# Performance work log

Measured on AMD Instinct MI355X. Metric: run time of the kernel, lower is better.

## Reference

```python
import jax, jax.numpy as jnp
import numpy as np

B, ST, SK, D, H, HD, MLP, BLK, NRAND = 2, 2048, 2048, 512, 8, 64, 2048, 64, 3


def _bigbird_block_mask(nq, nk, r, rng):
    """Block-level BigBird mask: 3-block window + global first/last blocks + r random blocks/row."""
    bm = np.zeros((nq, nk), dtype=bool)
    for i in range(nq):
        bm[i, max(i - 1, 0):min(i + 2, nk)] = True  # sliding window of 3 blocks
    bm[0, :] = True; bm[-1, :] = True              # global query blocks
    bm[:, 0] = True; bm[:, -1] = True              # global key blocks
    for i in range(nq):
        avail = np.where(~bm[i])[0]
        if avail.size:
            bm[i, rng.choice(avail, size=min(r, avail.size), replace=False)] = True
    return bm


def _masks():
    rng = np.random.RandomState(0)  # connectivity_seed = 0
    nb_q, nb_k = ST // BLK, SK // BLK
    self_bm = _bigbird_block_mask(nb_q, nb_q, NRAND, rng)
    cross_bm = _bigbird_block_mask(nb_q, nb_k, NRAND, rng)
    ones_blk = np.ones((BLK, BLK), dtype=bool)
    self_mask = np.kron(self_bm, ones_blk) & np.tril(np.ones((ST, ST), dtype=bool))  # causal self-attn
    cross_mask = np.kron(cross_bm, ones_blk)
    return jnp.asarray(self_mask), jnp.asarray(cross_mask)


def setup_inputs() -> dict:
    key = jax.random.key(0)
    ks = jax.random.split(key, 12)
    sd = np.float32(1.0 / np.sqrt(D))
    sh = np.float32(1.0 / np.sqrt(H * HD))
    sm = np.float32(1.0 / np.sqrt(MLP))
    self_mask, cross_mask = _masks()
    return dict(
        targets=jax.random.normal(ks[0], (B, ST, D), jnp.float32),
        encoded=jax.random.normal(ks[1], (B, SK, D), jnp.float32),
        ln1_scale=jnp.ones((D,), jnp.float32), ln1_bias=jnp.zeros((D,), jnp.float32),
        ln2_scale=jnp.ones((D,), jnp.float32), ln2_bias=jnp.zeros((D,), jnp.float32),
        ln3_scale=jnp.ones((D,), jnp.float32), ln3_bias=jnp.zeros((D,), jnp.float32),
        wq1=jax.random.normal(ks[2], (D, H, HD), jnp.float32) * sd,
        wk1=jax.random.normal(ks[3], (D, H, HD), jnp.float32) * sd,
        wv1=jax.random.normal(ks[4], (D, H, HD), jnp.float32) * sd,
        wo1=jax.random.normal(ks[5], (H, HD, D), jnp.float32) * sh,
        wq2=jax.random.normal(ks[6], (D, H, HD), jnp.float32) * sd,
        wk2=jax.random.normal(ks[7], (D, H, HD), jnp.float32) * sd,
        wv2=jax.random.normal(ks[8], (D, H, HD), jnp.float32) * sd,
        wo2=jax.random.normal(ks[9], (H, HD, D), jnp.float32) * sh,
        mlp_w1=jax.random.normal(ks[10], (D, MLP), jnp.float32) * sd,
        mlp_b1=jnp.zeros((MLP,), jnp.float32),
        mlp_w2=jax.random.normal(ks[11], (MLP, D), jnp.float32) * sm,
        mlp_b2=jnp.zeros((D,), jnp.float32),
        self_mask=self_mask, cross_mask=cross_mask,
    )


def _ln(x, s, b, eps=1e-6):
    mu = jnp.mean(x, axis=-1, keepdims=True)
    var = jnp.mean(jnp.square(x - mu), axis=-1, keepdims=True)
    return (x - mu) * jax.lax.rsqrt(var + eps) * s + b


def _attn(xq, xkv, wq, wk, wv, wo, mask):
    q = jnp.einsum('bsd,dhk->bshk', xq, wq) * np.float32(1.0 / np.sqrt(HD))
    k = jnp.einsum('bsd,dhk->bshk', xkv, wk)
    v = jnp.einsum('bsd,dhk->bshk', xkv, wv)
    scores = jnp.einsum('bqhd,bkhd->bhqk', q, k)
    scores = jnp.where(mask[None, None], scores, jnp.float32(-1e9))
    w = jax.nn.softmax(scores, axis=-1)
    o = jnp.einsum('bhqk,bkhd->bqhd', w, v)
    return jnp.einsum('bqhd,hdo->bqo', o, wo)


def reference(targets, encoded, ln1_scale, ln1_bias, ln2_scale, ln2_bias, ln3_scale, ln3_bias,
              wq1, wk1, wv1, wo1, wq2, wk2, wv2, wo2,
              mlp_w1, mlp_b1, mlp_w2, mlp_b2, self_mask, cross_mask):
    # causal BigBird self-attention + residual
    x = _ln(targets, ln1_scale, ln1_bias)
    x = _attn(x, x, wq1, wk1, wv1, wo1, self_mask) + targets
    # BigBird cross-attention over encoder output + residual
    y = _ln(x, ln2_scale, ln2_bias)
    y = _attn(y, encoded, wq2, wk2, wv2, wo2, cross_mask) + x
    # MLP block + residual
    z = _ln(y, ln3_scale, ln3_bias)
    z = jax.nn.gelu(z @ mlp_w1 + mlp_b1) @ mlp_w2 + mlp_b2
    return y + z
```

## Files before the change

### kernel.cpp

```cpp
#include <hip/hip_runtime.h>
#include <hip/hip_bf16.h>

#define DEVINL __device__ __forceinline__

namespace {

constexpr int kB = 2, kST = 2048, kSK = 2048, kD = 512, kH = 8, kHD = 64, kMLP = 2048, kBLK = 64;
constexpr int kNBQ = kST / kBLK;
constexpr int kNBK = kSK / kBLK;
constexpr int kROWS = kB * kST;
constexpr int kSPL = 8;

typedef float f32x4 __attribute__((ext_vector_type(4)));
typedef int i32x4 __attribute__((ext_vector_type(4)));
typedef short bf16x8 __attribute__((ext_vector_type(8)));

DEVINL float bf2f(unsigned short u) { return __uint_as_float(((unsigned)u) << 16); }

DEVINL unsigned short f2bf(float f) {
  __hip_bfloat16 h = __float2bfloat16(f);
  return *reinterpret_cast<unsigned short*>(&h);
}

DEVINL f32x4 mfma16(bf16x8 a, bf16x8 b, f32x4 c) {
  return __builtin_amdgcn_mfma_f32_16x16x32_bf16(a, b, c, 0, 0, 0);
}

DEVINL int swzb(int r) { return (((r & 7) ^ ((r >> 3) & 7)) << 4); }

__global__ __launch_bounds__(256) void tobf_kernel(const void* __restrict__ src, unsigned short* __restrict__ dst,
                                                   int n8, const unsigned* __restrict__ probe) {
  const bool bf = (probe[0] == 0x3F803F80u);
  const int stride = gridDim.x * blockDim.x;
  if (bf) {
    const i32x4* s = (const i32x4*)src;
    i32x4* d = (i32x4*)dst;
    for (int i = blockIdx.x * blockDim.x + threadIdx.x; i < n8; i += stride) d[i] = s[i];
  } else {
    const f32x4* s = (const f32x4*)src;
    i32x4* d = (i32x4*)dst;
    for (int i = blockIdx.x * blockDim.x + threadIdx.x; i < n8; i += stride) {
      const f32x4 a = s[2 * i], c = s[2 * i + 1];
      union { i32x4 v; unsigned short u[8]; } pk;
#pragma unroll
      for (int j = 0; j < 4; j++) { pk.u[j] = f2bf(a[j]); pk.u[4 + j] = f2bf(c[j]); }
      d[i] = pk.v;
    }
  }
}

struct PSrc { const void* s[8]; };
__global__ __launch_bounds__(256) void param_cvt_kernel(PSrc ps, float* __restrict__ dst,
                                                        const unsigned* __restrict__ probe) {
  const bool bf = (probe[0] == 0x3F803F80u);
  const int i = blockIdx.x * blockDim.x + threadIdx.x;
  if (i >= 5632) return;
  int seg, off;
  if (i < 3072) { seg = i >> 9; off = i & 511; }
  else if (i < 5120) { seg = 6; off = i - 3072; }
  else { seg = 7; off = i - 5120; }
  dst[i] = bf ? bf2f(((const unsigned short*)ps.s[seg])[off]) : ((const float*)ps.s[seg])[off];
}

struct TDesc { const void* src; unsigned short* dst; int K, N, start; float alpha; };
struct TPack { TDesc d[10]; };

__global__ __launch_bounds__(256) void transpose_batch_kernel(TPack p, const unsigned* __restrict__ probe) {
  __shared__ float tile[32][33];
  const bool bf = (probe[0] == 0x3F803F80u);
  const int bid = blockIdx.x;
  int di = 0;
#pragma unroll
  for (int i = 1; i < 10; i++)
    if (bid >= p.d[i].start) di = i;
  const TDesc dd = p.d[di];
  const int local = bid - dd.start;
  const int gx = dd.N / 32;
  const int bx = (local % gx) * 32;
  const int by = (local / gx) * 32;
  const int tx = threadIdx.x & 31, ty = threadIdx.x >> 5;
#pragma unroll
  for (int j = 0; j < 4; j++) {
    const int kr = by + ty + j * 8;
    float v;
    if (bf) v = bf2f(((const unsigned short*)dd.src)[(size_t)kr * dd.N + bx + tx]);
    else v = ((const float*)dd.src)[(size_t)kr * dd.N + bx + tx];
    tile[ty + j * 8][tx] = v;
  }
  __syncthreads();
#pragma unroll
  for (int j = 0; j < 4; j++) {
    const int nr = bx + ty + j * 8;
    dd.dst[(size_t)nr * dd.K + by + tx] = f2bf(dd.alpha * tile[tx][ty + j * 8]);
  }
}

DEVINL int mask_fmt(const void* self_mask) {
  const unsigned* sw = (const unsigned*)self_mask;
  unsigned w = sw[32256];
  unsigned w0 = sw[0];
  if (w == 0x01010101u) return 0;
  if (w0 == 0x3F800000u) return 2;
  if (w0 == 0x00003F80u) return 3;
  return 1;
}

DEVINL bool mask_at(const void* m, int r, int c, int fmt) {
  size_t idx = (size_t)r * kSK + c;
  switch (fmt) {
    case 0: return ((const unsigned char*)m)[idx] != 0;
    case 2: return ((const float*)m)[idx] != 0.f;
    case 3: return ((const unsigned short*)m)[idx] != 0;
    default: return ((const int*)m)[idx] != 0;
  }
}

__global__ void mask_kernel(const void* __restrict__ smask, const void* __restrict__ cmask,
                            unsigned char* __restrict__ sbm, unsigned char* __restrict__ cbm) {
  int fmt = mask_fmt(smask);
  int t = blockIdx.x * blockDim.x + threadIdx.x;
  if (t < kNBQ * kNBK) {
    int i = t / kNBK, j = t % kNBK;
    sbm[t] = mask_at(smask, i * kBLK + kBLK - 1, j * kBLK, fmt) ? 1 : 0;
    cbm[t] = mask_at(cmask, i * kBLK, j * kBLK, fmt) ? 1 : 0;
  }
}

__global__ __launch_bounds__(256) void ln_kernel(const void* __restrict__ x, const float* __restrict__ s,
                                                 const float* __restrict__ b, unsigned short* __restrict__ out,
                                                 int raw, const unsigned* __restrict__ probe) {
  const int row = blockIdx.x, t = threadIdx.x;
  float v0, v1;
  if (raw && probe[0] == 0x3F803F80u) {
    const unsigned u = ((const unsigned*)x)[(size_t)row * 256 + t];
    v0 = bf2f((unsigned short)u);
    v1 = bf2f((unsigned short)(u >> 16));
  } else {
    const float2 f = ((const float2*)x)[(size_t)row * 256 + t];
    v0 = f.x; v1 = f.y;
  }
  float sum = v0 + v1;
#pragma unroll
  for (int o = 32; o; o >>= 1) sum += __shfl_xor(sum, o);
  __shared__ float red[4], red2[4];
  const int wid = t >> 6, lane = t & 63;
  if (lane == 0) red[wid] = sum;
  __syncthreads();
  const float mu = (red[0] + red[1] + red[2] + red[3]) * (1.f / 512.f);
  float d0 = v0 - mu, d1 = v1 - mu;
  float vs = d0 * d0 + d1 * d1;
#pragma unroll
  for (int o = 32; o; o >>= 1) vs += __shfl_xor(vs, o);
  if (lane == 0) red2[wid] = vs;
  __syncthreads();
  const float rstd = rsqrtf((red2[0] + red2[1] + red2[2] + red2[3]) * (1.f / 512.f) + 1e-6f);
  const float o0 = d0 * rstd * s[2 * t] + b[2 * t];
  const float o1 = d1 * rstd * s[2 * t + 1] + b[2 * t + 1];
  ((unsigned*)out)[(size_t)row * 256 + t] = (unsigned)f2bf(o0) | ((unsigned)f2bf(o1) << 16);
}

DEVINL float gelu_f(float x) {
  float u = 0.7978845608028654f * (x + 0.044715f * x * x * x);
  return 0.5f * x * (1.f + tanhf(u));
}

enum { GEPI_QKV = 0, GEPI_QKV2 = 1, GEPI_RESID_RAW = 2, GEPI_RESID = 3, GEPI_GELU = 4, GEPI_FINAL = 5 };

template <int BM, int WM, int WN, int MT, int NT, int EPI>
__global__ __launch_bounds__(256) void mfma_gemm_kernel(
    const unsigned short* __restrict__ A, const unsigned short* __restrict__ A2,
    const unsigned short* __restrict__ Bt,
    void* __restrict__ Cout, int M, int N, int K,
    const float* __restrict__ bias, const void* __restrict__ resid,
    const unsigned* __restrict__ probe) {
  __shared__ __align__(16) unsigned short As[2][BM * 64];
  __shared__ __align__(16) unsigned short Bs[2][128 * 64];
  const int t = threadIdx.x, w = t >> 6, lane = t & 63;
  const int lg = lane >> 4, lc = lane & 15;
  const int wm = w / WN, wn = w % WN;
  const int bm = blockIdx.y * BM, bn = blockIdx.x * 128;

  const unsigned short* Aop = A;
  if constexpr (EPI == GEPI_QKV2) {
    if (bn >= 512) Aop = A2;
  }

  f32x4 acc[MT][NT];
#pragma unroll
  for (int mt = 0; mt < MT; mt++)
#pragma unroll
    for (int nt = 0; nt < NT; nt++) acc[mt][nt] = f32x4{0.f, 0.f, 0.f, 0.f};

  constexpr int AU = BM / 32;
  const int row0 = t >> 3, part16 = (t & 7) * 16;

  i32x4 ar[AU], br[4];
  auto LOADR = [&](int k0) {
#pragma unroll
    for (int i = 0; i < AU; i++) ar[i] = *(const i32x4*)(Aop + (size_t)(bm + row0 + i * 32) * K + k0 + (part16 >> 1));
#pragma unroll
    for (int i = 0; i < 4; i++) br[i] = *(const i32x4*)(Bt + (size_t)(bn + row0 + i * 32) * K + k0 + (part16 >> 1));
  };
  auto WRITES = [&](int buf) {
#pragma unroll
    for (int i = 0; i < AU; i++) {
      const int r = row0 + i * 32;
      *(i32x4*)((char*)&As[buf][0] + r * 128 + (part16 ^ swzb(r))) = ar[i];
    }
#pragma unroll
    for (int i = 0; i < 4; i++) {
      const int r = row0 + i * 32;
      *(i32x4*)((char*)&Bs[buf][0] + r * 128 + (part16 ^ swzb(r))) = br[i];
    }
  };
  auto COMPUTE = [&](int buf) {
#pragma unroll
    for (int c = 0; c < 2; c++) {
      bf16x8 af[MT], bfv[NT];
#pragma unroll
      for (int mt = 0; mt < MT; mt++) {
        const int r = wm * (MT * 16) + mt * 16 + lc;
        af[mt] = *(const bf16x8*)((const char*)&As[buf][0] + r * 128 + ((c * 64 + lg * 16) ^ swzb(r)));
      }
#pragma unroll
      for (int nt = 0; nt < NT; nt++) {
        const int r = wn * (NT * 16) + nt * 16 + lc;
        bfv[nt] = *(const bf16x8*)((const char*)&Bs[buf][0] + r * 128 + ((c * 64 + lg * 16) ^ swzb(r)));
      }
#pragma unroll
      for (int mt = 0; mt < MT; mt++)
#pragma unroll
        for (int nt = 0; nt < NT; nt++) acc[mt][nt] = mfma16(af[mt], bfv[nt], acc[mt][nt]);
    }
  };

  LOADR(0);
  WRITES(0);
  for (int k0 = 0; k0 < K; k0 += 128) {
    __syncthreads();
    LOADR(k0 + 64);
    COMPUTE(0);
    WRITES(1);
    __syncthreads();
    if (k0 + 128 < K) LOADR(k0 + 128);
    COMPUTE(1);
    if (k0 + 128 < K) WRITES(0);
  }

  bool prb = false;
  if constexpr (EPI == GEPI_FINAL || EPI == GEPI_RESID_RAW) prb = (probe[0] == 0x3F803F80u);
#pragma unroll
  for (int mt = 0; mt < MT; mt++) {
#pragma unroll
    for (int i = 0; i < 4; i++) {
      const int row = bm + wm * (MT * 16) + mt * 16 + lg * 4 + i;
#pragma unroll
      for (int nt = 0; nt < NT; nt++) {
        const int col = bn + wn * (NT * 16) + nt * 16 + lc;
        const float vv = acc[mt][nt][i];
        const size_t idx = (size_t)row * N + col;
        if constexpr (EPI == GEPI_QKV || EPI == GEPI_QKV2) {
          const int bb = row >> 11, ss = row & 2047;
          const int hh = (col >> 6) & 7, hd = col & 63;
          ((unsigned short*)Cout)[(size_t)(col >> 9) * kROWS * 512 +
                                  (((size_t)bb * kH + hh) * kST + ss) * 64 + hd] = f2bf(vv);
        } else if constexpr (EPI == GEPI_RESID_RAW) {
          const float rv = prb ? bf2f(((const unsigned short*)resid)[idx]) : ((const float*)resid)[idx];
          ((float*)Cout)[idx] = vv + rv;
        } else if constexpr (EPI == GEPI_RESID) {
          ((float*)Cout)[idx] = vv + ((const float*)resid)[idx];
        } else if constexpr (EPI == GEPI_GELU) {
          ((unsigned short*)Cout)[idx] = f2bf(gelu_f(vv + bias[col]));
        } else {
          const float r = vv + bias[col] + ((const float*)resid)[idx];
          if (prb) ((unsigned short*)Cout)[idx] = f2bf(r);
          else ((float*)Cout)[idx] = r;
        }
      }
    }
  }
}

template <bool CAUSAL>
__global__ __launch_bounds__(256) void attn_part_kernel(
    const unsigned short* __restrict__ q, const unsigned short* __restrict__ k,
    const unsigned short* __restrict__ v, const unsigned char* __restrict__ bm,
    unsigned short* __restrict__ opart, float* __restrict__ mpart, float* __restrict__ lpart) {
  __shared__ __align__(16) char smem[16384];
  const int x = blockIdx.x;
  const int s = x & 7, b = (x >> 3) & 1, qb = x >> 4;
  const int h = blockIdx.y;
  const int t = threadIdx.x, w = t >> 6, lane = t & 63;
  const int lg = lane >> 4, lc = lane & 15;

  const unsigned char* bmrow = bm + qb * kNBK;
  const unsigned mask = (unsigned)__ballot(lane < kNBK ? (bmrow[lane] != 0) : false);
  const int cnt = __popc(mask);
  const int lo = (s * cnt) >> 3, hi = ((s + 1) * cnt) >> 3;
  unsigned mrem = mask;
  for (int i = 0; i < lo; i++) mrem &= mrem - 1;
  const int left = hi - lo;

  const size_t hbase = ((size_t)b * kH + h) * kST;
  const size_t qbase = (hbase + qb * 64 + w * 16 + lc) * 64;
  const bf16x8 aq0 = *(const bf16x8*)(q + qbase + 8 * lg);
  const bf16x8 aq1 = *(const bf16x8*)(q + qbase + 32 + 8 * lg);

  f32x4 ob[4];
#pragma unroll
  for (int dt = 0; dt < 4; dt++) ob[dt] = f32x4{0.f, 0.f, 0.f, 0.f};
  float mi = -1e30f, li = 0.f;

  char* ksb = smem;
  char* vtb = smem + 8192;

  const int krr = t >> 3, kc16 = (t & 7) * 16;
  const int vkvp = t >> 3, vdc = (t & 7) * 8;
  const int vposb = ((vkvp >> 4) << 6) + (((vkvp >> 1) & 3) << 4) + (((vkvp >> 3) & 1) << 3) + ((vkvp & 1) << 2);

  i32x4 kr0, kr1, vr0, vr1;
  auto LOADT = [&](int j) {
    const unsigned short* kb = k + (hbase + j * 64) * 64;
    kr0 = *(const i32x4*)(kb + t * 8);
    kr1 = *(const i32x4*)(kb + 2048 + t * 8);
    const unsigned short* vb = v + (hbase + j * 64) * 64;
    vr0 = *(const i32x4*)(vb + (2 * vkvp) * 64 + vdc);
    vr1 = *(const i32x4*)(vb + (2 * vkvp + 1) * 64 + vdc);
  };
  auto WRITET = [&]() {
    *(i32x4*)(ksb + krr * 128 + (kc16 ^ swzb(krr))) = kr0;
    *(i32x4*)(ksb + (krr + 32) * 128 + (kc16 ^ swzb(krr + 32))) = kr1;
    union { i32x4 v4; unsigned short u[8]; } a0, a1;
    a0.v4 = vr0; a1.v4 = vr1;
#pragma unroll
    for (int jj = 0; jj < 8; jj++) {
      const int d = vdc + jj;
      const unsigned val = (unsigned)a0.u[jj] | ((unsigned)a1.u[jj] << 16);
      *(unsigned*)(vtb + d * 128 + (vposb ^ swzb(d))) = val;
    }
  };

  if (left > 0) {
    int jcur = (int)__builtin_ctz(mrem);
    mrem &= mrem - 1;
    LOADT(jcur);
    WRITET();
    for (int r = 0; r < left; r++) {
      int jnext = -1;
      if (r + 1 < left) { jnext = (int)__builtin_ctz(mrem); mrem &= mrem - 1; }
      __syncthreads();
      if (jnext >= 0) LOADT(jnext);

      f32x4 sv[4];
#pragma unroll
      for (int t4 = 0; t4 < 4; t4++) sv[t4] = f32x4{0.f, 0.f, 0.f, 0.f};
#pragma unroll
      for (int c = 0; c < 2; c++) {
        const bf16x8 aqc = c ? aq1 : aq0;
#pragma unroll
        for (int t4 = 0; t4 < 4; t4++) {
          const int row = t4 * 16 + lc;
          bf16x8 bk = *(const bf16x8*)(ksb + row * 128 + ((c * 64 + lg * 16) ^ swzb(row)));
          sv[t4] = mfma16(bk, aqc, sv[t4]);
        }
      }

      if (CAUSAL && jcur == qb) {
#pragma unroll
        for (int t4 = 0; t4 < 4; t4++)
#pragma unroll
          for (int i = 0; i < 4; i++)
            if (t4 * 16 + lg * 4 + i > w * 16 + lc) sv[t4][i] = -1e30f;
      }

      float pm = sv[0][0];
#pragma unroll
      for (int t4 = 0; t4 < 4; t4++)
#pragma unroll
        for (int i = 0; i < 4; i++) pm = fmaxf(pm, sv[t4][i]);
      pm = fmaxf(pm, __shfl_xor(pm, 16));
      pm = fmaxf(pm, __shfl_xor(pm, 32));
      const float mn = fmaxf(mi, pm);
      const float corr = __expf(mi - mn);
      mi = mn;
      float rs = 0.f;
#pragma unroll
      for (int t4 = 0; t4 < 4; t4++)
#pragma unroll
        for (int i = 0; i < 4; i++) {
          sv[t4][i] = __expf(sv[t4][i] - mn);
          rs += sv[t4][i];
        }
      rs += __shfl_xor(rs, 16);
      rs += __shfl_xor(rs, 32);
      li = li * corr + rs;

      float cb[4];
#pragma unroll
      for (int i = 0; i < 4; i++) cb[i] = __shfl(corr, lg * 4 + i);
#pragma unroll
      for (int dt = 0; dt < 4; dt++)
#pragma unroll
        for (int i = 0; i < 4; i++) ob[dt][i] *= cb[i];

      bf16x8 pa[2];
#pragma unroll
      for (int c = 0; c < 2; c++) {
        union { bf16x8 v8; unsigned short u[8]; } pk;
#pragma unroll
        for (int jj = 0; jj < 8; jj++) pk.u[jj] = f2bf(sv[2 * c + (jj >> 2)][jj & 3]);
        pa[c] = pk.v8;
      }
#pragma unroll
      for (int c = 0; c < 2; c++)
#pragma unroll
        for (int dt = 0; dt < 4; dt++) {
          const int row = dt * 16 + lc;
          bf16x8 bv = *(const bf16x8*)(vtb + row * 128 + ((c * 64 + lg * 16) ^ swzb(row)));
          ob[dt] = mfma16(pa[c], bv, ob[dt]);
        }

      __syncthreads();
      if (jnext >= 0) WRITET();
      jcur = jnext;
    }
  }

  const int pidx = ((((b * kNBQ + qb) * kH) + h)) * kSPL + s;
  unsigned short* op = opart + (size_t)pidx * 4096;
#pragma unroll
  for (int dt = 0; dt < 4; dt++)
#pragma unroll
    for (int i = 0; i < 4; i++)
      op[(w * 16 + lg * 4 + i) * 64 + dt * 16 + lc] = f2bf(ob[dt][i]);
  if (lg == 0) {
    mpart[pidx * 64 + w * 16 + lc] = mi;
    lpart[pidx * 64 + w * 16 + lc] = li;
  }
}

__global__ __launch_bounds__(256) void attn_comb_kernel(
    const unsigned short* __restrict__ opart, const float* __restrict__ mpart,
    const float* __restrict__ lpart, unsigned short* __restrict__ o) {
  const int x = blockIdx.x;
  const int qb = x >> 1, b = x & 1, h = blockIdx.y;
  const int t = threadIdx.x;
  const int base = ((((b * kNBQ + qb) * kH) + h)) * kSPL;
  const int r = t >> 2, cg = (t & 3) * 16;
  float m[kSPL], l[kSPL];
#pragma unroll
  for (int s = 0; s < kSPL; s++) {
    m[s] = mpart[(base + s) * 64 + r];
    l[s] = lpart[(base + s) * 64 + r];
  }
  float M = m[0];
#pragma unroll
  for (int s = 1; s < kSPL; s++) M = fmaxf(M, m[s]);
  float wgt[kSPL], L = 0.f;
#pragma unroll
  for (int s = 0; s < kSPL; s++) {
    wgt[s] = __expf(m[s] - M);
    L += l[s] * wgt[s];
  }
  const float inv = 1.f / L;
  float val[16];
#pragma unroll
  for (int c = 0; c < 16; c++) val[c] = 0.f;
#pragma unroll
  for (int s = 0; s < kSPL; s++) {
    const unsigned short* op = opart + (size_t)(base + s) * 4096 + r * 64 + cg;
    union { i32x4 v; unsigned short u[8]; } lo_, hi_;
    lo_.v = *(const i32x4*)op;
    hi_.v = *(const i32x4*)(op + 8);
#pragma unroll
    for (int c = 0; c < 8; c++) {
      val[c] += bf2f(lo_.u[c]) * wgt[s];
      val[8 + c] += bf2f(hi_.u[c]) * wgt[s];
    }
  }
  const size_t ob_ = (((size_t)b * kST + qb * 64 + r) * kH + h) * kHD + cg;
#pragma unroll
  for (int c = 0; c < 16; c++) o[ob_ + c] = f2bf(val[c] * inv);
}

}

extern "C" void kernel_launch(void* const* d_in, const int* in_sizes, int n_in,
                              void* d_out, int out_size, void* d_ws, size_t ws_size,
                              hipStream_t stream) {
  (void)in_sizes; (void)n_in; (void)out_size; (void)ws_size;
  const unsigned* probe = (const unsigned*)d_in[2];

  char* W = (char*)d_ws;
  size_t off = 0;
  auto allocb = [&](size_t bytes) { char* p = W + off; off += (bytes + 255) & ~size_t(255); return p; };

  float* xbuf = (float*)allocb((size_t)kROWS * kD * 4);
  float* ybuf = (float*)allocb((size_t)kROWS * kD * 4);
  float* f_par = (float*)allocb(5632 * 4);
  float* f_ln[6];
  for (int i = 0; i < 6; i++) f_ln[i] = f_par + i * 512;
  float* f_b1 = f_par + 3072;
  float* f_b2 = f_par + 5120;
  unsigned short* encb = (unsigned short*)allocb((size_t)kROWS * kD * 2);
  unsigned short* lnb  = (unsigned short*)allocb((size_t)kROWS * kD * 2);
  unsigned short* qkvb = (unsigned short*)allocb((size_t)3 * kROWS * kD * 2);
  unsigned short* qkv2 = (unsigned short*)allocb((size_t)3 * kROWS * kD * 2);
  unsigned short* aob  = (unsigned short*)allocb((size_t)kROWS * kD * 2);
  unsigned short* hb16 = (unsigned short*)allocb((size_t)kROWS * kMLP * 2);
  unsigned short* wqkv1 = (unsigned short*)allocb((size_t)3 * 512 * 512 * 2);
  unsigned short* wqkv2 = (unsigned short*)allocb((size_t)3 * 512 * 512 * 2);
  unsigned short* wo1t  = (unsigned short*)allocb((size_t)512 * 512 * 2);
  unsigned short* wo2t  = (unsigned short*)allocb((size_t)512 * 512 * 2);
  unsigned short* w1t   = (unsigned short*)allocb((size_t)2048 * 512 * 2);
  unsigned short* w2t   = (unsigned short*)allocb((size_t)512 * 2048 * 2);
  unsigned char* sbm = (unsigned char*)allocb(kNBQ * kNBK);
  unsigned char* cbm = (unsigned char*)allocb(kNBQ * kNBK);
  unsigned short* opart = (unsigned short*)allocb((size_t)512 * kSPL * 4096 * 2);
  float* mpart = (float*)allocb((size_t)512 * kSPL * 64 * 4);
  float* lpart = (float*)allocb((size_t)512 * kSPL * 64 * 4);

  tobf_kernel<<<1024, 256, 0, stream>>>(d_in[1], encb, kROWS * kD / 8, probe);
  {
    PSrc ps;
    for (int i = 0; i < 6; i++) ps.s[i] = d_in[2 + i];
    ps.s[6] = d_in[17];
    ps.s[7] = d_in[19];
    param_cvt_kernel<<<22, 256, 0, stream>>>(ps, f_par, probe);
  }
  {
    TPack p;
    const void* srcs[10] = {d_in[8], d_in[9], d_in[10],
                            d_in[12], d_in[13], d_in[14],
                            d_in[11], d_in[15], d_in[16], d_in[18]};
    unsigned short* dsts[10] = {wqkv1, wqkv1 + 512 * 512, wqkv1 + 2 * 512 * 512,
                                wqkv2, wqkv2 + 512 * 512, wqkv2 + 2 * 512 * 512,
                                wo1t, wo2t, w1t, w2t};
    const int Ksz[10] = {512, 512, 512, 512, 512, 512, 512, 512, 512, 2048};
    const int Nsz[10] = {512, 512, 512, 512, 512, 512, 512, 512, 2048, 512};
    int start = 0;
    for (int i = 0; i < 10; i++) {
      p.d[i].src = srcs[i]; p.d[i].dst = dsts[i]; p.d[i].K = Ksz[i]; p.d[i].N = Nsz[i];
      p.d[i].start = start;
      p.d[i].alpha = (i == 0 || i == 3) ? 0.125f : 1.0f;
      start += (Nsz[i] / 32) * (Ksz[i] / 32);
    }
    transpose_batch_kernel<<<start, 256, 0, stream>>>(p, probe);
  }
  mask_kernel<<<1, 1024, 0, stream>>>(d_in[20], d_in[21], sbm, cbm);

  const dim3 blk(256);
  const dim3 g_qkv(12, 32);
  const dim3 g_mlp1(16, 32);
  const dim3 g_n512(4, 64);
  const dim3 g_attnp(kNBQ * kB * kSPL, kH);
  const dim3 g_attnc(kNBQ * kB, kH);

  unsigned short* qb16 = qkvb;
  unsigned short* kb16 = qkvb + (size_t)kROWS * 512;
  unsigned short* vb16 = qkvb + (size_t)2 * kROWS * 512;
  unsigned short* q2b = qkv2;
  unsigned short* k2b = qkv2 + (size_t)kROWS * 512;
  unsigned short* v2b = qkv2 + (size_t)2 * kROWS * 512;

  ln_kernel<<<kROWS, blk, 0, stream>>>(d_in[0], f_ln[0], f_ln[1], lnb, 1, probe);
  mfma_gemm_kernel<128, 2, 2, 4, 4, GEPI_QKV><<<g_qkv, blk, 0, stream>>>(lnb, nullptr, wqkv1, qkvb, kROWS, 1536, 512, nullptr, nullptr, probe);
  attn_part_kernel<true><<<g_attnp, blk, 0, stream>>>(qb16, kb16, vb16, sbm, opart, mpart, lpart);
  attn_comb_kernel<<<g_attnc, blk, 0, stream>>>(opart, mpart, lpart, aob);
  mfma_gemm_kernel<64, 1, 4, 4, 2, GEPI_RESID_RAW><<<g_n512, blk, 0, stream>>>(aob, nullptr, wo1t, xbuf, kROWS, 512, 512, nullptr, d_in[0], probe);

  ln_kernel<<<kROWS, blk, 0, stream>>>(xbuf, f_ln[2], f_ln[3], lnb, 0, probe);
  mfma_gemm_kernel<128, 2, 2, 4, 4, GEPI_QKV2><<<g_qkv, blk, 0, stream>>>(lnb, encb, wqkv2, qkv2, kROWS, 1536, 512, nullptr, nullptr, probe);
  attn_part_kernel<false><<<g_attnp, blk, 0, stream>>>(q2b, k2b, v2b, cbm, opart, mpart, lpart);
  attn_comb_kernel<<<g_attnc, blk, 0, stream>>>(opart, mpart, lpart, aob);
  mfma_gemm_kernel<64, 1, 4, 4, 2, GEPI_RESID><<<g_n512, blk, 0, stream>>>(aob, nullptr, wo2t, ybuf, kROWS, 512, 512, nullptr, xbuf, probe);

  ln_kernel<<<kROWS, blk, 0, stream>>>(ybuf, f_ln[4], f_ln[5], lnb, 0, probe);
  mfma_gemm_kernel<128, 2, 2, 4, 4, GEPI_GELU><<<g_mlp1, blk, 0, stream>>>(lnb, nullptr, w1t, hb16, kROWS, kMLP, 512, f_b1, nullptr, probe);
  mfma_gemm_kernel<64, 1, 4, 4, 2, GEPI_FINAL><<<g_n512, blk, 0, stream>>>(hb16, nullptr, w2t, d_out, kROWS, 512, 2048, f_b2, ybuf, probe);
}
```

Measured before the change: 209.4 us.

## Merge prologue conversion kernels into one launch and swizzle GEMM workgroup order

Four setup kernels (encoder bf16 conversion, parameter conversion, weight transposes, block-mask extraction) are folded into a single prologue kernel that dispatches on block index. This removes three kernel launches and their serialization gaps. The GEMM kernel also remaps its flat workgroup index with a stride-8 permutation, so that consecutively dispatched workgroups spread across XCDs/tiles and get better L2 locality. The remap assumes the workgroup count divides by 8, which holds for the grids used.

Result: faster. 200.1 us (-4.4%).

```diff
diff --git a/kernel.cpp b/kernel.cpp
--- a/kernel.cpp
+++ b/kernel.cpp
@@ -28,72 +28,19 @@
 
 DEVINL int swzb(int r) { return (((r & 7) ^ ((r >> 3) & 7)) << 4); }
 
-__global__ __launch_bounds__(256) void tobf_kernel(const void* __restrict__ src, unsigned short* __restrict__ dst,
-                                                   int n8, const unsigned* __restrict__ probe) {
-  const bool bf = (probe[0] == 0x3F803F80u);
-  const int stride = gridDim.x * blockDim.x;
-  if (bf) {
-    const i32x4* s = (const i32x4*)src;
-    i32x4* d = (i32x4*)dst;
-    for (int i = blockIdx.x * blockDim.x + threadIdx.x; i < n8; i += stride) d[i] = s[i];
-  } else {
-    const f32x4* s = (const f32x4*)src;
-    i32x4* d = (i32x4*)dst;
-    for (int i = blockIdx.x * blockDim.x + threadIdx.x; i < n8; i += stride) {
-      const f32x4 a = s[2 * i], c = s[2 * i + 1];
-      union { i32x4 v; unsigned short u[8]; } pk;
-#pragma unroll
-      for (int j = 0; j < 4; j++) { pk.u[j] = f2bf(a[j]); pk.u[4 + j] = f2bf(c[j]); }
-      d[i] = pk.v;
-    }
-  }
-}
-
-struct PSrc { const void* s[8]; };
-__global__ __launch_bounds__(256) void param_cvt_kernel(PSrc ps, float* __restrict__ dst,
-                                                        const unsigned* __restrict__ probe) {
-  const bool bf = (probe[0] == 0x3F803F80u);
-  const int i = blockIdx.x * blockDim.x + threadIdx.x;
-  if (i >= 5632) return;
-  int seg, off;
-  if (i < 3072) { seg = i >> 9; off = i & 511; }
-  else if (i < 5120) { seg = 6; off = i - 3072; }
-  else { seg = 7; off = i - 5120; }
-  dst[i] = bf ? bf2f(((const unsigned short*)ps.s[seg])[off]) : ((const float*)ps.s[seg])[off];
-}
-
 struct TDesc { const void* src; unsigned short* dst; int K, N, start; float alpha; };
-struct TPack { TDesc d[10]; };
-
-__global__ __launch_bounds__(256) void transpose_batch_kernel(TPack p, const unsigned* __restrict__ probe) {
-  __shared__ float tile[32][33];
-  const bool bf = (probe[0] == 0x3F803F80u);
-  const int bid = blockIdx.x;
-  int di = 0;
-#pragma unroll
-  for (int i = 1; i < 10; i++)
-    if (bid >= p.d[i].start) di = i;
-  const TDesc dd = p.d[di];
-  const int local = bid - dd.start;
-  const int gx = dd.N / 32;
-  const int bx = (local % gx) * 32;
-  const int by = (local / gx) * 32;
-  const int tx = threadIdx.x & 31, ty = threadIdx.x >> 5;
-#pragma unroll
-  for (int j = 0; j < 4; j++) {
-    const int kr = by + ty + j * 8;
-    float v;
-    if (bf) v = bf2f(((const unsigned short*)dd.src)[(size_t)kr * dd.N + bx + tx]);
-    else v = ((const float*)dd.src)[(size_t)kr * dd.N + bx + tx];
-    tile[ty + j * 8][tx] = v;
-  }
-  __syncthreads();
-#pragma unroll
-  for (int j = 0; j < 4; j++) {
-    const int nr = bx + ty + j * 8;
-    dd.dst[(size_t)nr * dd.K + by + tx] = f2bf(dd.alpha * tile[tx][ty + j * 8]);
-  }
-}
+struct Pro {
+  TDesc d[10];
+  const void* enc_src;
+  unsigned short* enc_dst;
+  const void* ps[8];
+  float* par_dst;
+  const void* smask;
+  const void* cmask;
+  unsigned char* sbm;
+  unsigned char* cbm;
+};
+constexpr int kProT = 4096, kProTobf = 5120, kProPar = 5142, kProN = 5143;
 
 DEVINL int mask_fmt(const void* self_mask) {
   const unsigned* sw = (const unsigned*)self_mask;
@@ -115,14 +62,66 @@
   }
 }
 
-__global__ void mask_kernel(const void* __restrict__ smask, const void* __restrict__ cmask,
-                            unsigned char* __restrict__ sbm, unsigned char* __restrict__ cbm) {
-  int fmt = mask_fmt(smask);
-  int t = blockIdx.x * blockDim.x + threadIdx.x;
-  if (t < kNBQ * kNBK) {
-    int i = t / kNBK, j = t % kNBK;
-    sbm[t] = mask_at(smask, i * kBLK + kBLK - 1, j * kBLK, fmt) ? 1 : 0;
-    cbm[t] = mask_at(cmask, i * kBLK, j * kBLK, fmt) ? 1 : 0;
+__global__ __launch_bounds__(256) void prologue_kernel(Pro p, const unsigned* __restrict__ probe) {
+  __shared__ float tile[32][33];
+  const bool bf = (probe[0] == 0x3F803F80u);
+  const int bid = blockIdx.x;
+  const int tid = threadIdx.x;
+
+  if (bid < kProT) {
+    int di = 0;
+#pragma unroll
+    for (int i = 1; i < 10; i++)
+      if (bid >= p.d[i].start) di = i;
+    const TDesc dd = p.d[di];
+    const int local = bid - dd.start;
+    const int gx = dd.N / 32;
+    const int bx = (local % gx) * 32;
+    const int by = (local / gx) * 32;
+    const int tx = tid & 31, ty = tid >> 5;
+#pragma unroll
+    for (int j = 0; j < 4; j++) {
+      const int kr = by + ty + j * 8;
+      float v;
+      if (bf) v = bf2f(((const unsigned short*)dd.src)[(size_t)kr * dd.N + bx + tx]);
+      else v = ((const float*)dd.src)[(size_t)kr * dd.N + bx + tx];
+      tile[ty + j * 8][tx] = v;
+    }
+    __syncthreads();
+#pragma unroll
+    for (int j = 0; j < 4; j++) {
+      const int nr = bx + ty + j * 8;
+      dd.dst[(size_t)nr * dd.K + by + tx] = f2bf(dd.alpha * tile[tx][ty + j * 8]);
+    }
+  } else if (bid < kProTobf) {
+    const int i = (bid - kProT) * 256 + tid;
+    if (bf) {
+      ((i32x4*)p.enc_dst)[i] = ((const i32x4*)p.enc_src)[i];
+    } else {
+      const f32x4 a = ((const f32x4*)p.enc_src)[2 * i];
+      const f32x4 c = ((const f32x4*)p.enc_src)[2 * i + 1];
+      union { i32x4 v; unsigned short u[8]; } pk;
+#pragma unroll
+      for (int j = 0; j < 4; j++) { pk.u[j] = f2bf(a[j]); pk.u[4 + j] = f2bf(c[j]); }
+      ((i32x4*)p.enc_dst)[i] = pk.v;
+    }
+  } else if (bid < kProPar) {
+    const int i = (bid - kProTobf) * 256 + tid;
+    if (i < 5632) {
+      int seg, off;
+      if (i < 3072) { seg = i >> 9; off = i & 511; }
+      else if (i < 5120) { seg = 6; off = i - 3072; }
+      else { seg = 7; off = i - 5120; }
+      p.par_dst[i] = bf ? bf2f(((const unsigned short*)p.ps[seg])[off]) : ((const float*)p.ps[seg])[off];
+    }
+  } else {
+    const int fmt = mask_fmt(p.smask);
+    for (int it = 0; it < 4; it++) {
+      const int t = it * 256 + tid;
+      const int i = t / kNBK, j = t % kNBK;
+      p.sbm[t] = mask_at(p.smask, i * kBLK + kBLK - 1, j * kBLK, fmt) ? 1 : 0;
+      p.cbm[t] = mask_at(p.cmask, i * kBLK, j * kBLK, fmt) ? 1 : 0;
+    }
   }
 }
 
@@ -178,7 +177,11 @@
   const int t = threadIdx.x, w = t >> 6, lane = t & 63;
   const int lg = lane >> 4, lc = lane & 15;
   const int wm = w / WN, wn = w % WN;
-  const int bm = blockIdx.y * BM, bn = blockIdx.x * 128;
+
+  const int nwg = gridDim.x * gridDim.y;
+  int flat = blockIdx.y * gridDim.x + blockIdx.x;
+  flat = (flat & 7) * (nwg >> 3) + (flat >> 3);
+  const int bm = (flat / gridDim.x) * BM, bn = (flat % gridDim.x) * 128;
 
   const unsigned short* Aop = A;
   if constexpr (EPI == GEPI_QKV2) {
@@ -520,16 +523,8 @@
   float* mpart = (float*)allocb((size_t)512 * kSPL * 64 * 4);
   float* lpart = (float*)allocb((size_t)512 * kSPL * 64 * 4);
 
-  tobf_kernel<<<1024, 256, 0, stream>>>(d_in[1], encb, kROWS * kD / 8, probe);
   {
-    PSrc ps;
-    for (int i = 0; i < 6; i++) ps.s[i] = d_in[2 + i];
-    ps.s[6] = d_in[17];
-    ps.s[7] = d_in[19];
-    param_cvt_kernel<<<22, 256, 0, stream>>>(ps, f_par, probe);
-  }
-  {
-    TPack p;
+    Pro p;
     const void* srcs[10] = {d_in[8], d_in[9], d_in[10],
                             d_in[12], d_in[13], d_in[14],
                             d_in[11], d_in[15], d_in[16], d_in[18]};
@@ -545,9 +540,16 @@
       p.d[i].alpha = (i == 0 || i == 3) ? 0.125f : 1.0f;
       start += (Nsz[i] / 32) * (Ksz[i] / 32);
     }
-    transpose_batch_kernel<<<start, 256, 0, stream>>>(p, probe);
-  }
-  mask_kernel<<<1, 1024, 0, stream>>>(d_in[20], d_in[21], sbm, cbm);
+    p.enc_src = d_in[1];
+    p.enc_dst = encb;
+    for (int i = 0; i < 6; i++) p.ps[i] = d_in[2 + i];
+    p.ps[6] = d_in[17];
+    p.ps[7] = d_in[19];
+    p.par_dst = f_par;
+    p.smask = d_in[20]; p.cmask = d_in[21];
+    p.sbm = sbm; p.cbm = cbm;
+    prologue_kernel<<<kProN, 256, 0, stream>>>(p, probe);
+  }
 
   const dim3 blk(256);
   const dim3 g_qkv(12, 32);
```
